# Kernel optimization log

Hardware: AMD Instinct MI355X
Metric: run time of the kernel (lower is better)

## Reference

```python
import jax, jax.numpy as jnp
import numpy as np

B, N, P = 8, 4096, 1024
P4 = P // 4
EPS = 1e-5


def _ln(x, g, b):
    mu = jnp.mean(x, axis=-1, keepdims=True)
    var = jnp.var(x, axis=-1, keepdims=True)
    return (x - mu) * jax.lax.rsqrt(var + EPS) * g + b


def setup_inputs() -> dict:
    key = jax.random.key(0)
    ks = jax.random.split(key, 16)
    s = lambda fan: 1.0 / np.sqrt(fan)
    return {
        "xyz": jax.random.normal(ks[0], (B, N, 3), jnp.float32),
        "x": jax.random.normal(ks[1], (B, N, P), jnp.float32),
        "ln1_g": jnp.ones((P,), jnp.float32),
        "ln1_b": jnp.zeros((P,), jnp.float32),
        "ln2_g": jnp.ones((P,), jnp.float32),
        "ln2_b": jnp.zeros((P,), jnp.float32),
        "qk_w": jax.random.normal(ks[2], (P4, P), jnp.float32) * s(P),   # shared q/k 1x1 conv, no bias
        "v_w": jax.random.normal(ks[3], (P, P), jnp.float32) * s(P),
        "v_b": jax.random.normal(ks[4], (P,), jnp.float32) * s(P),
        "t1_w": jax.random.normal(ks[5], (P, P4), jnp.float32) * s(P4),  # trans_conv
        "t1_b": jax.random.normal(ks[6], (P,), jnp.float32) * s(P4),
        "t2_w": jax.random.normal(ks[7], (P, P4), jnp.float32) * s(P4),  # trans_conv1
        "t2_b": jax.random.normal(ks[8], (P,), jnp.float32) * s(P4),
        "m1_w": jax.random.normal(ks[9], (P, P), jnp.float32) * s(P),
        "m1_b": jax.random.normal(ks[10], (P,), jnp.float32) * s(P),
        "m2_w": jax.random.normal(ks[11], (P, P), jnp.float32) * s(P),
        "m2_b": jax.random.normal(ks[12], (P,), jnp.float32) * s(P),
    }


def reference(xyz, x, ln1_g, ln1_b, ln2_g, ln2_b, qk_w, v_w, v_b,
              t1_w, t1_b, t2_w, t2_b, m1_w, m1_b, m2_w, m2_b):
    # xyz is accepted but unused, matching the torch module. Dropout = eval identity.
    res1 = x
    h = _ln(x, ln1_g, ln1_b)                                   # [B,N,P]
    # TransformerBlock_1 (1x1 convs on h^T [B,P,N] are just matmuls over P)
    x_q = jnp.einsum('op,bnp->bon', qk_w, h)                   # [B,P4,N]
    # k shares weights with q; x_k permuted is x_q transposed
    x_v = jnp.einsum('op,bnp->bno', v_w, h) + v_b              # [B,N,P]
    energy = jnp.einsum('bqn,bkn->bqk', x_q, x_q)              # [B,P4,P4]
    att = jnp.einsum('op,bpk->bok', t1_w, energy) + t1_b[:, None]   # [B,P,P4]
    att = jax.nn.gelu(att, approximate=False)
    att = jnp.einsum('op,bkp->bok', t2_w, att) + t2_b[:, None]      # [B,P,P]
    att = jax.nn.softmax(att, axis=-1)
    t_out = jnp.einsum('bnp,bpq->bnq', x_v, att)               # [B,N,P]
    x1 = t_out + res1
    h2 = _ln(x1, ln2_g, ln2_b)
    m = jax.nn.gelu(h2 @ m1_w.T + m1_b, approximate=False)
    m = m @ m2_w.T + m2_b
    return x1 + m
```

## Files before the change

kernel.cpp:

```cpp
#include <hip/hip_runtime.h>


typedef __attribute__((ext_vector_type(4))) float f32x4;
typedef __attribute__((ext_vector_type(8))) _Float16 h16x8;
typedef __attribute__((ext_vector_type(8))) unsigned short u16x8;
typedef __attribute__((ext_vector_type(4))) unsigned short u16x4;

__device__ __forceinline__ unsigned short f2h(float f) {
  _Float16 h = (_Float16)f;
  return __builtin_bit_cast(unsigned short, h);
}
__device__ __forceinline__ float h2f(unsigned short u) {
  return (float)__builtin_bit_cast(_Float16, u);
}
__device__ __forceinline__ unsigned split16(float f) {
  _Float16 h = (_Float16)f;
  _Float16 l = (_Float16)(f - (float)h);
  return (unsigned)__builtin_bit_cast(unsigned short, h) |
         ((unsigned)__builtin_bit_cast(unsigned short, l) << 16);
}
__device__ __forceinline__ float gelu_f(float x) {
  return 0.5f * x * (1.0f + erff(x * 0.70710678118654752f));
}
__device__ __forceinline__ void gload16(const void* g, void* l) {
  __builtin_amdgcn_global_load_lds(
      (const __attribute__((address_space(1))) unsigned int*)g,
      (__attribute__((address_space(3))) unsigned int*)l, 16, 0, 0);
}
#define FENCE() asm volatile("" ::: "memory")

__device__ __forceinline__ void xcd_swz(int& bx, int& by, int gx, int gy) {
  const int nwg = gx * gy;
  if ((nwg & 7) == 0 && nwg >= 16) {
    const int flat = bx + gx * by;
    const int chunk = nwg >> 3;
    const int nf = (flat & 7) * chunk + (flat >> 3);
    bx = nf % gx;
    by = nf / gx;
  }
}

__global__ __launch_bounds__(256)
void ln_kernel(const float* __restrict__ x, const float* __restrict__ g,
               const float* __restrict__ b, unsigned short* __restrict__ hi,
               unsigned short* __restrict__ lo, unsigned short* __restrict__ xh) {
  __shared__ float red[16];
  const size_t base = (size_t)blockIdx.x * 1024;
  const int t = threadIdx.x;
  f32x4 v = *(const f32x4*)&x[base + t * 4];
  float s = v[0] + v[1] + v[2] + v[3];
  float q = v[0] * v[0] + v[1] * v[1] + v[2] * v[2] + v[3] * v[3];
#pragma unroll
  for (int o = 32; o > 0; o >>= 1) { s += __shfl_down(s, o); q += __shfl_down(q, o); }
  const int w = t >> 6;
  if ((t & 63) == 0) { red[w] = s; red[8 + w] = q; }
  __syncthreads();
  s = (red[0] + red[1]) + (red[2] + red[3]);
  q = (red[8] + red[9]) + (red[10] + red[11]);
  const float mu = s * (1.0f / 1024.0f);
  const float var = q * (1.0f / 1024.0f) - mu * mu;
  const float is = rsqrtf(var + 1e-5f);
  f32x4 gg = *(const f32x4*)&g[t * 4];
  f32x4 bb = *(const f32x4*)&b[t * 4];
  u16x4 oh, ol, ox;
#pragma unroll
  for (int j = 0; j < 4; j++) {
    float y = (v[j] - mu) * is * gg[j] + bb[j];
    unsigned p = split16(y);
    oh[j] = (unsigned short)(p & 0xffffu);
    ol[j] = (unsigned short)(p >> 16);
    ox[j] = f2h(v[j]);
  }
  *(u16x4*)&hi[base + t * 4] = oh;
  if (lo) *(u16x4*)&lo[base + t * 4] = ol;
  if (xh) *(u16x4*)&xh[base + t * 4] = ox;
}

__global__ __launch_bounds__(256)
void stats16_kernel(const unsigned short* __restrict__ x16, float* __restrict__ muis) {
  __shared__ float red[16];
  const size_t base = (size_t)blockIdx.x * 1024;
  const int t = threadIdx.x;
  u16x4 raw = *(const u16x4*)&x16[base + t * 4];
  float v[4];
#pragma unroll
  for (int j = 0; j < 4; j++) v[j] = h2f(raw[j]);
  float s = v[0] + v[1] + v[2] + v[3];
  float q = v[0] * v[0] + v[1] * v[1] + v[2] * v[2] + v[3] * v[3];
#pragma unroll
  for (int o = 32; o > 0; o >>= 1) { s += __shfl_down(s, o); q += __shfl_down(q, o); }
  const int w = t >> 6;
  if ((t & 63) == 0) { red[w] = s; red[8 + w] = q; }
  __syncthreads();
  if (t == 0) {
    s = (red[0] + red[1]) + (red[2] + red[3]);
    q = (red[8] + red[9]) + (red[10] + red[11]);
    const float mu = s * (1.0f / 1024.0f);
    const float var = q * (1.0f / 1024.0f) - mu * mu;
    muis[blockIdx.x * 2] = mu;
    muis[blockIdx.x * 2 + 1] = rsqrtf(var + 1e-5f);
  }
}

__global__ __launch_bounds__(256)
void cvt_kernel(const float* __restrict__ in, unsigned short* __restrict__ hi,
                unsigned short* __restrict__ lo, int n4) {
  int i = blockIdx.x * 256 + threadIdx.x;
  if (i < n4) {
    f32x4 v = *(const f32x4*)&in[(size_t)i * 4];
    u16x4 oh, ol;
#pragma unroll
    for (int j = 0; j < 4; j++) {
      unsigned p = split16(v[j]);
      oh[j] = (unsigned short)(p & 0xffffu);
      ol[j] = (unsigned short)(p >> 16);
    }
    *(u16x4*)&hi[(size_t)i * 4] = oh;
    if (lo) *(u16x4*)&lo[(size_t)i * 4] = ol;
  }
}

__global__ __launch_bounds__(256)
void m1prep_kernel(const float* __restrict__ m1w, const float* __restrict__ lng,
                   const float* __restrict__ lnb, const float* __restrict__ m1b,
                   unsigned short* __restrict__ wp, float* __restrict__ S,
                   float* __restrict__ b2) {
  __shared__ float red[16];
  const int o = blockIdx.x;
  const int t = threadIdx.x;
  const float* row = m1w + (size_t)o * 1024;
  f32x4 wv = *(const f32x4*)&row[t * 4];
  f32x4 gv = *(const f32x4*)&lng[t * 4];
  f32x4 bv = *(const f32x4*)&lnb[t * 4];
  float s = 0.0f, d = 0.0f;
  u16x4 ow;
#pragma unroll
  for (int j = 0; j < 4; j++) {
    float wpj = wv[j] * gv[j];
    ow[j] = f2h(wpj);
    s += wpj;
    d += wv[j] * bv[j];
  }
  *(u16x4*)&wp[(size_t)o * 1024 + t * 4] = ow;
#pragma unroll
  for (int off = 32; off > 0; off >>= 1) { s += __shfl_down(s, off); d += __shfl_down(d, off); }
  const int w = t >> 6;
  if ((t & 63) == 0) { red[w] = s; red[8 + w] = d; }
  __syncthreads();
  if (t == 0) {
    S[o] = (red[0] + red[1]) + (red[2] + red[3]);
    b2[o] = m1b[o] + (red[8] + red[9]) + (red[10] + red[11]);
  }
}

__global__ __launch_bounds__(256)
void vwt_kernel(const float* __restrict__ vw, unsigned short* __restrict__ wvt) {
  __shared__ float T[64][65];
  const int bx = blockIdx.x, by = blockIdx.y;
  const int t = threadIdx.x;
  const int lr = t >> 6, lc = t & 63;
#pragma unroll
  for (int i = 0; i < 16; ++i) {
    const int row = i * 4 + lr;
    T[row][lc] = vw[(size_t)(by * 64 + row) * 1024 + bx * 64 + lc];
  }
  __syncthreads();
#pragma unroll
  for (int i = 0; i < 16; ++i) {
    const int row = i * 4 + lr;
    wvt[(size_t)(bx * 64 + row) * 1024 + by * 64 + lc] = f2h(T[lc][row]);
  }
}

__global__ __launch_bounds__(256)
void beff_kernel(const unsigned short* __restrict__ attT, const float* __restrict__ vb,
                 float* __restrict__ beff) {
  const int b = blockIdx.y;
  const int q = blockIdx.x * 4 + (threadIdx.x >> 6);
  const int l = threadIdx.x & 63;
  const unsigned short* row = attT + ((size_t)b * 1024 + q) * 1024;
  float s = 0.0f;
#pragma unroll
  for (int i = 0; i < 2; ++i) {
    u16x8 v = *(const u16x8*)&row[(i * 64 + l) * 8];
    f32x4 vb0 = *(const f32x4*)&vb[(i * 64 + l) * 8];
    f32x4 vb1 = *(const f32x4*)&vb[(i * 64 + l) * 8 + 4];
#pragma unroll
    for (int j = 0; j < 4; j++) s += h2f(v[j]) * vb0[j];
#pragma unroll
    for (int j = 0; j < 4; j++) s += h2f(v[j + 4]) * vb1[j];
  }
#pragma unroll
  for (int o = 32; o > 0; o >>= 1) s += __shfl_down(s, o);
  if (l == 0) beff[b * 1024 + q] = s;
}

template <int EPI>
__global__ __launch_bounds__(256)
void gemm_v(const unsigned short* __restrict__ Ain, const unsigned short* __restrict__ Bin,
            void* __restrict__ Cout, const float* __restrict__ bias,
            const unsigned short* __restrict__ res16In, const float* __restrict__ muis,
            const float* __restrict__ Svec,
            int K, int lda, int ldb, int ldc,
            long long sA, long long sB, long long sC, long long sBias, long long sRes) {
  __shared__ short As[2][4096];
  __shared__ short Bs[2][4096];
  const int z = blockIdx.z;
  const unsigned short* A = Ain + (size_t)z * sA;
  const unsigned short* B = Bin + (size_t)z * sB;
  int bx = blockIdx.x, by = blockIdx.y;
  xcd_swz(bx, by, gridDim.x, gridDim.y);
  const int mBase = by * 128, nBase = bx * 128;
  const int t = threadIdx.x, w = t >> 6, l = t & 63;
  const int r16 = l & 15, kq = l >> 4;
  const int wr = (w >> 1) * 64, wc = (w & 1) * 64;
  f32x4 acc[4][4] = {};

  auto stage = [&](int buf, int k0) {
#pragma unroll
    for (int i = 0; i < 2; ++i) {
      const int c = i * 256 + t;
      const int row = c >> 2, cc = c & 3;
      const int gc = cc ^ ((row >> 1) & 3);
      short* la = &As[buf][(i * 256 + w * 64) * 8];
      short* lb = &Bs[buf][(i * 256 + w * 64) * 8];
      gload16(&A[(size_t)(mBase + row) * lda + k0 + gc * 8], la);
      gload16(&B[(size_t)(nBase + row) * ldb + k0 + gc * 8], lb);
    }
  };

  const int nt = K >> 5;
  stage(0, 0);
  if (nt > 1) stage(1, 32);
  for (int ts = 0; ts < nt; ++ts) {
    const int cur = ts & 1;
    if (ts + 1 < nt) { asm volatile("s_waitcnt vmcnt(4)" ::: "memory"); }
    else             { asm volatile("s_waitcnt vmcnt(0)" ::: "memory"); }
    __builtin_amdgcn_s_barrier();
    FENCE();
    h16x8 aF[4], bF[4];
#pragma unroll
    for (int mi = 0; mi < 4; mi++) {
      const int r = wr + mi * 16 + r16;
      aF[mi] = *(const h16x8*)&As[cur][r * 32 + (kq ^ ((r >> 1) & 3)) * 8];
    }
#pragma unroll
    for (int ni = 0; ni < 4; ni++) {
      const int r = wc + ni * 16 + r16;
      bF[ni] = *(const h16x8*)&Bs[cur][r * 32 + (kq ^ ((r >> 1) & 3)) * 8];
    }
    __builtin_amdgcn_s_setprio(1);
#pragma unroll
    for (int mi = 0; mi < 4; mi++)
#pragma unroll
      for (int ni = 0; ni < 4; ni++)
        acc[mi][ni] = __builtin_amdgcn_mfma_f32_16x16x32_f16(aF[mi], bF[ni], acc[mi][ni], 0, 0, 0);
    __builtin_amdgcn_s_setprio(0);
    FENCE();
    __builtin_amdgcn_s_barrier();
    FENCE();
    if (ts + 2 < nt) stage(cur, (ts + 2) * 32);
  }
  FENCE();

  unsigned short* C16 = (unsigned short*)Cout + (size_t)z * sC;
  float* C32 = (float*)Cout + (size_t)z * sC;
  const float* bp = (EPI != 4) ? bias + (size_t)z * sBias : nullptr;
  const unsigned short* rp = (EPI == 3) ? res16In + (size_t)z * sRes : nullptr;

  if constexpr (EPI == 1 || EPI == 4 || EPI == 9) {
    short* ep = ((w & 2) ? &Bs[0][0] : &As[0][0]) + (w & 1) * 4096;
#pragma unroll
    for (int mi = 0; mi < 4; mi++) {
      float mu[4], is[4];
      if (EPI == 9) {
#pragma unroll
        for (int r = 0; r < 4; r++) {
          const int rw = mBase + wr + mi * 16 + kq * 4 + r;
          mu[r] = muis[rw * 2];
          is[r] = muis[rw * 2 + 1];
        }
      }
#pragma unroll
      for (int ni = 0; ni < 4; ni++) {
        const int cl = nBase + wc + ni * 16 + r16;
        const float bcol = bp ? bp[cl] : 0.0f;
        const float Scol = (EPI == 9) ? Svec[cl] : 0.0f;
#pragma unroll
        for (int r = 0; r < 4; r++) {
          float v;
          if (EPI == 9) v = gelu_f(is[r] * (acc[mi][ni][r] - mu[r] * Scol) + bcol);
          else {
            v = acc[mi][ni][r] + bcol;
            if (EPI == 1) v = gelu_f(v);
          }
          ep[(mi * 16 + kq * 4 + r) * 64 + ni * 16 + r16] = (short)f2h(v);
        }
      }
    }
#pragma unroll
    for (int j = 0; j < 8; j++) {
      const int f = j * 512 + l * 8;
      const int row = f >> 6, col = f & 63;
      const size_t gi = (size_t)(mBase + wr + row) * ldc + nBase + wc + col;
      *(u16x8*)&C16[gi] = *(const u16x8*)&ep[f];
    }
  } else {
#pragma unroll
    for (int mi = 0; mi < 4; mi++) {
#pragma unroll
      for (int ni = 0; ni < 4; ni++) {
        const int cl = nBase + wc + ni * 16 + r16;
        const float bcol = bp[cl];
#pragma unroll
        for (int r = 0; r < 4; r++) {
          const int rw = mBase + wr + mi * 16 + kq * 4 + r;
          const size_t idx = (size_t)rw * ldc + cl;
          C32[idx] = acc[mi][ni][r] + bcol + h2f(rp[idx]);
        }
      }
    }
  }
}

__global__ __launch_bounds__(256)
void gemm_r(const unsigned short* __restrict__ Ain, const unsigned short* __restrict__ Bin,
            unsigned short* __restrict__ Cout, const float* __restrict__ bias,
            const unsigned short* __restrict__ resIn,
            int K, int lda, int ldb, int ldc,
            long long sA, long long sB, long long sC, long long sBias, long long sRes) {
  __shared__ short As[2][4096];
  __shared__ short Bs[2][4096];
  const int z = blockIdx.z;
  const unsigned short* A = Ain + (size_t)z * sA;
  const unsigned short* B = Bin + (size_t)z * sB;
  int bx = blockIdx.x, by = blockIdx.y;
  xcd_swz(bx, by, gridDim.x, gridDim.y);
  const int mBase = by * 128, nBase = bx * 128;
  const int t = threadIdx.x, w = t >> 6, l = t & 63;
  const int r16 = l & 15, kq = l >> 4;
  const int wr = (w >> 1) * 64, wc = (w & 1) * 64;
  f32x4 acc[4][4] = {};

  const int row0 = t >> 2, row1 = 64 + (t >> 2);
  const int cc0 = t & 3;
  const int gc0 = cc0 ^ ((row0 >> 1) & 3);
  const int gc1 = cc0 ^ ((row1 >> 1) & 3);

  u16x8 ra0, ra1, rb0, rb1;
  auto loadreg = [&](int k0) {
    ra0 = *(const u16x8*)&A[(size_t)(mBase + row0) * lda + k0 + gc0 * 8];
    rb0 = *(const u16x8*)&B[(size_t)(nBase + row0) * ldb + k0 + gc0 * 8];
    ra1 = *(const u16x8*)&A[(size_t)(mBase + row1) * lda + k0 + gc1 * 8];
    rb1 = *(const u16x8*)&B[(size_t)(nBase + row1) * ldb + k0 + gc1 * 8];
  };
  auto dswrite = [&](int buf) {
    *(u16x8*)&As[buf][t * 8] = ra0;
    *(u16x8*)&Bs[buf][t * 8] = rb0;
    *(u16x8*)&As[buf][(256 + t) * 8] = ra1;
    *(u16x8*)&Bs[buf][(256 + t) * 8] = rb1;
  };

  const int nt = K >> 5;
  loadreg(0);
  dswrite(0);
  if (nt > 1) loadreg(32);
  asm volatile("s_waitcnt lgkmcnt(0)" ::: "memory");
  __builtin_amdgcn_s_barrier();
  FENCE();
  for (int ts = 0; ts < nt; ++ts) {
    const int cur = ts & 1;
    h16x8 aF[4], bF[4];
#pragma unroll
    for (int mi = 0; mi < 4; mi++) {
      const int r = wr + mi * 16 + r16;
      aF[mi] = *(const h16x8*)&As[cur][r * 32 + (kq ^ ((r >> 1) & 3)) * 8];
    }
#pragma unroll
    for (int ni = 0; ni < 4; ni++) {
      const int r = wc + ni * 16 + r16;
      bF[ni] = *(const h16x8*)&Bs[cur][r * 32 + (kq ^ ((r >> 1) & 3)) * 8];
    }
    __builtin_amdgcn_s_setprio(1);
#pragma unroll
    for (int mi = 0; mi < 4; mi++)
#pragma unroll
      for (int ni = 0; ni < 4; ni++)
        acc[mi][ni] = __builtin_amdgcn_mfma_f32_16x16x32_f16(aF[mi], bF[ni], acc[mi][ni], 0, 0, 0);
    __builtin_amdgcn_s_setprio(0);
    FENCE();
    if (ts + 1 < nt) {
      __builtin_amdgcn_s_barrier();
      FENCE();
      dswrite((ts + 1) & 1);
      if (ts + 2 < nt) loadreg((ts + 2) * 32);
      asm volatile("s_waitcnt lgkmcnt(0)" ::: "memory");
      FENCE();
      __builtin_amdgcn_s_barrier();
      FENCE();
    }
  }
  FENCE();

  unsigned short* C16 = Cout + (size_t)z * sC;
  const float* bp = bias + (size_t)z * sBias;
  const unsigned short* rp = resIn + (size_t)z * sRes;
  short* ep = ((w & 2) ? &Bs[0][0] : &As[0][0]) + (w & 1) * 4096;
#pragma unroll
  for (int mi = 0; mi < 4; mi++) {
#pragma unroll
    for (int ni = 0; ni < 4; ni++) {
      const int cl = nBase + wc + ni * 16 + r16;
      const float bcol = bp[cl];
#pragma unroll
      for (int r = 0; r < 4; r++)
        ep[(mi * 16 + kq * 4 + r) * 64 + ni * 16 + r16] =
            (short)f2h(acc[mi][ni][r] + bcol);
    }
  }
#pragma unroll
  for (int j = 0; j < 8; j++) {
    const int f = j * 512 + l * 8;
    const int row = f >> 6, col = f & 63;
    u16x8 v8 = *(const u16x8*)&ep[f];
    const size_t gi = (size_t)(mBase + wr + row) * ldc + nBase + wc + col;
    u16x8 r8 = *(const u16x8*)&rp[gi];
#pragma unroll
    for (int q = 0; q < 8; q++) v8[q] = f2h(h2f(v8[q]) + h2f(r8[q]));
    *(u16x8*)&C16[gi] = v8;
  }
}

template <int EPI, int SWAP>
__global__ __launch_bounds__(256)
void gemm_s(const unsigned short* __restrict__ Ahi, const unsigned short* __restrict__ Alo,
            const unsigned short* __restrict__ Bhi, const unsigned short* __restrict__ Blo,
            void* __restrict__ Cout, unsigned short* __restrict__ Cout2,
            const float* __restrict__ bias,
            int K, int lda, int ldb, int ldc,
            long long sA, long long sB, long long sC, int splitK) {
  __shared__ short As[2][8192];
  __shared__ short Bs[2][8192];
  const int z = blockIdx.z;
  const int bi = z / splitK, sp = z % splitK;
  const int kLen = K / splitK, kStart = sp * kLen;
  const unsigned short* AH = Ahi + (size_t)bi * sA;
  const unsigned short* BH = Bhi + (size_t)bi * sB;
  const unsigned short* AL = Alo + (size_t)bi * sA;
  const unsigned short* BL = Blo + (size_t)bi * sB;
  int bx = blockIdx.x, by = blockIdx.y;
  xcd_swz(bx, by, gridDim.x, gridDim.y);
  const int mBase = (SWAP ? bx : by) * 128, nBase = (SWAP ? by : bx) * 128;
  const int t = threadIdx.x, w = t >> 6, l = t & 63;
  const int r16 = l & 15, kq = l >> 4;
  const int wr = (w >> 1) * 64, wc = (w & 1) * 64;
  f32x4 acc[4][4] = {};

  auto stage = [&](int buf, int k0) {
#pragma unroll
    for (int i = 0; i < 2; ++i) {
      const int c = i * 256 + t;
      const int row = c >> 2, cc = c & 3;
      const int gc = cc ^ ((row >> 1) & 3);
      const int cbase = i * 256 + w * 64;
      const size_t ga = (size_t)(mBase + row) * lda + k0 + gc * 8;
      const size_t gb = (size_t)(nBase + row) * ldb + k0 + gc * 8;
      gload16(&AH[ga], &As[buf][cbase * 8]);
      gload16(&AL[ga], &As[buf][4096 + cbase * 8]);
      gload16(&BH[gb], &Bs[buf][cbase * 8]);
      gload16(&BL[gb], &Bs[buf][4096 + cbase * 8]);
    }
  };

  const int nsteps = kLen >> 5;
  stage(0, kStart);
  if (nsteps > 1) stage(1, kStart + 32);
  for (int ts = 0; ts < nsteps; ++ts) {
    const int cur = ts & 1;
    if (ts + 1 < nsteps) { asm volatile("s_waitcnt vmcnt(8)" ::: "memory"); }
    else                 { asm volatile("s_waitcnt vmcnt(0)" ::: "memory"); }
    __builtin_amdgcn_s_barrier();
    FENCE();
    h16x8 aH[4], bH[4], aL[4], bL[4];
#pragma unroll
    for (int mi = 0; mi < 4; mi++) {
      const int r = wr + mi * 16 + r16;
      const int off = r * 32 + (kq ^ ((r >> 1) & 3)) * 8;
      aH[mi] = *(const h16x8*)&As[cur][off];
      aL[mi] = *(const h16x8*)&As[cur][4096 + off];
    }
#pragma unroll
    for (int ni = 0; ni < 4; ni++) {
      const int r = wc + ni * 16 + r16;
      const int off = r * 32 + (kq ^ ((r >> 1) & 3)) * 8;
      bH[ni] = *(const h16x8*)&Bs[cur][off];
      bL[ni] = *(const h16x8*)&Bs[cur][4096 + off];
    }
    __builtin_amdgcn_s_setprio(1);
#pragma unroll
    for (int mi = 0; mi < 4; mi++)
#pragma unroll
      for (int ni = 0; ni < 4; ni++) {
        acc[mi][ni] = __builtin_amdgcn_mfma_f32_16x16x32_f16(aH[mi], bH[ni], acc[mi][ni], 0, 0, 0);
        acc[mi][ni] = __builtin_amdgcn_mfma_f32_16x16x32_f16(aH[mi], bL[ni], acc[mi][ni], 0, 0, 0);
        acc[mi][ni] = __builtin_amdgcn_mfma_f32_16x16x32_f16(aL[mi], bH[ni], acc[mi][ni], 0, 0, 0);
      }
    __builtin_amdgcn_s_setprio(0);
    FENCE();
    __builtin_amdgcn_s_barrier();
    FENCE();
    if (ts + 2 < nsteps) stage(cur, kStart + (ts + 2) * 32);
  }
  FENCE();

  unsigned short* C16 = (unsigned short*)Cout + (size_t)z * sC;
  unsigned short* C16b = Cout2 ? Cout2 + (size_t)z * sC : nullptr;
  float* C32 = (float*)Cout + (size_t)z * sC;

  if constexpr (EPI == 4 || EPI == 6) {
    short* ep = &As[0][0] + w * 4096;
    unsigned pk[4][4][4];
#pragma unroll
    for (int mi = 0; mi < 4; mi++)
#pragma unroll
      for (int ni = 0; ni < 4; ni++)
#pragma unroll
        for (int r = 0; r < 4; r++) {
          float v = acc[mi][ni][r];
          if (EPI == 6) { v += bias[mBase + wr + mi * 16 + kq * 4 + r]; v = gelu_f(v); }
          pk[mi][ni][r] = split16(v);
        }
#pragma unroll
    for (int mi = 0; mi < 4; mi++)
#pragma unroll
      for (int ni = 0; ni < 4; ni++)
#pragma unroll
        for (int r = 0; r < 4; r++)
          ep[(mi * 16 + kq * 4 + r) * 64 + ni * 16 + r16] =
              (short)(pk[mi][ni][r] & 0xffffu);
#pragma unroll
    for (int j = 0; j < 8; j++) {
      const int f = j * 512 + l * 8;
      const int row = f >> 6, col = f & 63;
      *(u16x8*)&C16[(size_t)(mBase + wr + row) * ldc + nBase + wc + col] =
          *(const u16x8*)&ep[f];
    }
#pragma unroll
    for (int mi = 0; mi < 4; mi++)
#pragma unroll
      for (int ni = 0; ni < 4; ni++)
#pragma unroll
        for (int r = 0; r < 4; r++)
          ep[(mi * 16 + kq * 4 + r) * 64 + ni * 16 + r16] =
              (short)(pk[mi][ni][r] >> 16);
#pragma unroll
    for (int j = 0; j < 8; j++) {
      const int f = j * 512 + l * 8;
      const int row = f >> 6, col = f & 63;
      *(u16x8*)&C16b[(size_t)(mBase + wr + row) * ldc + nBase + wc + col] =
          *(const u16x8*)&ep[f];
    }
  } else {
#pragma unroll
    for (int mi = 0; mi < 4; mi++) {
#pragma unroll
      for (int ni = 0; ni < 4; ni++) {
        const int cl = nBase + wc + ni * 16 + r16;
#pragma unroll
        for (int r = 0; r < 4; r++) {
          const int rw = mBase + wr + mi * 16 + kq * 4 + r;
          float v = acc[mi][ni][r];
          if (EPI == 7) v += bias[rw];
          C32[(size_t)rw * ldc + cl] = v;
        }
      }
    }
  }
}

__global__ __launch_bounds__(256)
void ereduce_kernel(const float* __restrict__ part, unsigned short* __restrict__ ehi,
                    unsigned short* __restrict__ elo) {
  const size_t idx = (size_t)blockIdx.x * 256 + threadIdx.x;
  const size_t b = idx >> 16, i = idx & 65535;
  const float* p = part + b * (8ull * 65536) + i;
  float s0 = (p[0] + p[65536]) + (p[2 * 65536] + p[3 * 65536]);
  float s1 = (p[4 * 65536] + p[5 * 65536]) + (p[6 * 65536] + p[7 * 65536]);
  unsigned pk = split16(s0 + s1);
  ehi[idx] = (unsigned short)(pk & 0xffffu);
  elo[idx] = (unsigned short)(pk >> 16);
}

__global__ __launch_bounds__(256)
void smax_t_kernel(const float* __restrict__ a2, unsigned short* __restrict__ attT) {
  __shared__ float S[8][1028];
  __shared__ float inv[8];
  const int t = threadIdx.x;
  const int b = blockIdx.y;
  const int o0 = blockIdx.x * 8;
  const float* src = a2 + ((size_t)b * 1024 + o0) * 1024;
#pragma unroll
  for (int i = 0; i < 8; i++)
    *(f32x4*)&S[i][t * 4] = *(const f32x4*)&src[(size_t)i * 1024 + t * 4];
  __syncthreads();
  const int w = t >> 6, l = t & 63;
  for (int rr = 0; rr < 2; rr++) {
    const int r = w * 2 + rr;
    float m = -1e30f;
#pragma unroll
    for (int i = 0; i < 16; i++) m = fmaxf(m, S[r][l + i * 64]);
#pragma unroll
    for (int o = 32; o > 0; o >>= 1) m = fmaxf(m, __shfl_xor(m, o));
    float ssum = 0.0f;
#pragma unroll
    for (int i = 0; i < 16; i++) {
      float e = expf(S[r][l + i * 64] - m);
      S[r][l + i * 64] = e;
      ssum += e;
    }
#pragma unroll
    for (int o = 32; o > 0; o >>= 1) ssum += __shfl_xor(ssum, o);
    if (l == 0) inv[r] = 1.0f / ssum;
  }
  __syncthreads();
  float iv[8];
#pragma unroll
  for (int r = 0; r < 8; r++) iv[r] = inv[r];
#pragma unroll
  for (int i = 0; i < 4; i++) {
    const int k = i * 256 + t;
    u16x8 ov;
#pragma unroll
    for (int r = 0; r < 8; r++) ov[r] = f2h(S[r][k] * iv[r]);
    *(u16x8*)&attT[((size_t)b * 1024 + k) * 1024 + o0] = ov;
  }
}

extern "C" void kernel_launch(void* const* d_in, const int* in_sizes, int n_in,
                              void* d_out, int out_size, void* d_ws, size_t ws_size,
                              hipStream_t stream) {
  (void)in_sizes; (void)n_in; (void)out_size; (void)ws_size;
  const float* x     = (const float*)d_in[1];
  const float* ln1_g = (const float*)d_in[2];
  const float* ln1_b = (const float*)d_in[3];
  const float* ln2_g = (const float*)d_in[4];
  const float* ln2_b = (const float*)d_in[5];
  const float* qk_w  = (const float*)d_in[6];
  const float* v_w   = (const float*)d_in[7];
  const float* v_b   = (const float*)d_in[8];
  const float* t1_w  = (const float*)d_in[9];
  const float* t1_b  = (const float*)d_in[10];
  const float* t2_w  = (const float*)d_in[11];
  const float* t2_b  = (const float*)d_in[12];
  const float* m1_w  = (const float*)d_in[13];
  const float* m1_b  = (const float*)d_in[14];
  const float* m2_w  = (const float*)d_in[15];
  const float* m2_b  = (const float*)d_in[16];

  char* ws = (char*)d_ws;
  unsigned short* hhi  = (unsigned short*)(ws + 0);
  unsigned short* hlo  = (unsigned short*)(ws + 67108864);
  unsigned short* Qthi = (unsigned short*)(ws + 134217728);
  unsigned short* Qtlo = (unsigned short*)(ws + 150994944);
  float*          part = (float*)(ws + 167772160);
  unsigned short* Ehi  = (unsigned short*)(ws + 184549376);
  unsigned short* Elo  = (unsigned short*)(ws + 185597952);
  unsigned short* Ghi  = (unsigned short*)(ws + 186646528);
  unsigned short* Glo  = (unsigned short*)(ws + 190840832);
  float*          a2   = (float*)(ws + 195035136);
  unsigned short* attT = (unsigned short*)(ws + 228589568);
  unsigned short* WeT  = (unsigned short*)(ws + 245366784);
  float*          beff = (float*)(ws + 262144000);
  float*          muis = (float*)(ws + 262176768);
  float*          Svec = (float*)(ws + 262438912);
  float*          b2   = (float*)(ws + 262443008);
  unsigned short* xh   = (unsigned short*)(ws + 268435456);
  unsigned short* x1h  = (unsigned short*)(ws + 335544320);
  unsigned short* wqh  = (unsigned short*)(ws + 446693376);
  unsigned short* wql  = (unsigned short*)(ws + 447217664);
  unsigned short* wvt  = (unsigned short*)(ws + 447741952);
  unsigned short* wt1h = (unsigned short*)(ws + 449839104);
  unsigned short* wt1l = (unsigned short*)(ws + 450363392);
  unsigned short* wt2h = (unsigned short*)(ws + 450887680);
  unsigned short* wt2l = (unsigned short*)(ws + 451411968);
  unsigned short* wm1p = (unsigned short*)(ws + 451936256);
  unsigned short* wm2  = (unsigned short*)(ws + 454033408);
  unsigned short* gb = hlo;
  float* out = (float*)d_out;

  cvt_kernel<<<dim3(256),  dim3(256), 0, stream>>>(qk_w, wqh, wql, 65536);
  vwt_kernel<<<dim3(16, 16), dim3(256), 0, stream>>>(v_w, wvt);
  cvt_kernel<<<dim3(256),  dim3(256), 0, stream>>>(t1_w, wt1h, wt1l, 65536);
  cvt_kernel<<<dim3(256),  dim3(256), 0, stream>>>(t2_w, wt2h, wt2l, 65536);
  m1prep_kernel<<<dim3(1024), dim3(256), 0, stream>>>(m1_w, ln2_g, ln2_b, m1_b, wm1p, Svec, b2);
  cvt_kernel<<<dim3(1024), dim3(256), 0, stream>>>(m2_w, wm2, nullptr, 262144);
  ln_kernel<<<dim3(32768), dim3(256), 0, stream>>>(x, ln1_g, ln1_b, hhi, hlo, xh);
  gemm_s<4, 1><<<dim3(2, 32, 8), dim3(256), 0, stream>>>(
      wqh, wql, hhi, hlo, Qthi, Qtlo, nullptr,
      1024, 1024, 1024, 4096, 0, 4194304, 1048576, 1);
  gemm_s<5, 0><<<dim3(2, 2, 64), dim3(256), 0, stream>>>(
      Qthi, Qtlo, Qthi, Qtlo, part, nullptr, nullptr,
      4096, 4096, 4096, 256, 1048576, 1048576, 65536, 8);
  ereduce_kernel<<<dim3(2048), dim3(256), 0, stream>>>(part, Ehi, Elo);
  gemm_s<6, 0><<<dim3(2, 8, 8), dim3(256), 0, stream>>>(
      wt1h, wt1l, Ehi, Elo, Ghi, Glo, t1_b,
      256, 256, 256, 256, 0, 65536, 262144, 1);
  gemm_s<7, 0><<<dim3(8, 8, 8), dim3(256), 0, stream>>>(
      wt2h, wt2l, Ghi, Glo, a2, nullptr, t2_b,
      256, 256, 256, 1024, 0, 262144, 1048576, 1);
  smax_t_kernel<<<dim3(128, 8), dim3(256), 0, stream>>>(a2, attT);
  gemm_v<4><<<dim3(8, 8, 8), dim3(256), 0, stream>>>(
      attT, wvt, WeT, nullptr, nullptr, nullptr, nullptr,
      1024, 1024, 1024, 1024, 1048576, 0, 1048576, 0, 0);
  beff_kernel<<<dim3(256, 8), dim3(256), 0, stream>>>(attT, v_b, beff);
  gemm_r<<<dim3(8, 32, 8), dim3(256), 0, stream>>>(
      hhi, WeT, x1h, beff, xh,
      1024, 1024, 1024, 1024, 4194304, 1048576, 4194304, 1024, 4194304);
  stats16_kernel<<<dim3(32768), dim3(256), 0, stream>>>(x1h, muis);
  gemm_v<9><<<dim3(8, 256, 1), dim3(256), 0, stream>>>(
      x1h, wm1p, gb, b2, nullptr, muis, Svec,
      1024, 1024, 1024, 1024, 0, 0, 0, 0, 0);
  gemm_v<3><<<dim3(8, 256, 1), dim3(256), 0, stream>>>(
      gb, wm2, out, m2_b, x1h, nullptr, nullptr,
      1024, 1024, 1024, 1024, 0, 0, 0, 0, 0);
}
```

Before: 634.8 us.

## Fold LayerNorm1 into Q and V GEMM epilogues via per-row stats

Replaces the materialized LN1 output with a raw split-fp16 copy of x plus per-row mean/inv-std, folding gamma into the Q and V weights and applying mean/scale corrections in the GEMM epilogues. The separate fp16 copy of x used as residual is dropped, and the residual now reads from the hi half of x. This removes writing the LN output and the xh buffer. The trade-off is extra epilogue arithmetic, extra prep kernels, and possible precision loss from cancellation in the mean-subtraction done after the matmul.

```diff
diff --git a/kernel.cpp b/kernel.cpp
--- a/kernel.cpp
+++ b/kernel.cpp
@@ -41,9 +41,8 @@
 }
 
 __global__ __launch_bounds__(256)
-void ln_kernel(const float* __restrict__ x, const float* __restrict__ g,
-               const float* __restrict__ b, unsigned short* __restrict__ hi,
-               unsigned short* __restrict__ lo, unsigned short* __restrict__ xh) {
+void lnsplit_kernel(const float* __restrict__ x, unsigned short* __restrict__ xhi,
+                    unsigned short* __restrict__ xlo, float* __restrict__ muis) {
   __shared__ float red[16];
   const size_t base = (size_t)blockIdx.x * 1024;
   const int t = threadIdx.x;
@@ -54,26 +53,24 @@
   for (int o = 32; o > 0; o >>= 1) { s += __shfl_down(s, o); q += __shfl_down(q, o); }
   const int w = t >> 6;
   if ((t & 63) == 0) { red[w] = s; red[8 + w] = q; }
-  __syncthreads();
-  s = (red[0] + red[1]) + (red[2] + red[3]);
-  q = (red[8] + red[9]) + (red[10] + red[11]);
-  const float mu = s * (1.0f / 1024.0f);
-  const float var = q * (1.0f / 1024.0f) - mu * mu;
-  const float is = rsqrtf(var + 1e-5f);
-  f32x4 gg = *(const f32x4*)&g[t * 4];
-  f32x4 bb = *(const f32x4*)&b[t * 4];
-  u16x4 oh, ol, ox;
+  u16x4 oh, ol;
 #pragma unroll
   for (int j = 0; j < 4; j++) {
-    float y = (v[j] - mu) * is * gg[j] + bb[j];
-    unsigned p = split16(y);
+    unsigned p = split16(v[j]);
     oh[j] = (unsigned short)(p & 0xffffu);
     ol[j] = (unsigned short)(p >> 16);
-    ox[j] = f2h(v[j]);
-  }
-  *(u16x4*)&hi[base + t * 4] = oh;
-  if (lo) *(u16x4*)&lo[base + t * 4] = ol;
-  if (xh) *(u16x4*)&xh[base + t * 4] = ox;
+  }
+  *(u16x4*)&xhi[base + t * 4] = oh;
+  *(u16x4*)&xlo[base + t * 4] = ol;
+  __syncthreads();
+  if (t == 0) {
+    s = (red[0] + red[1]) + (red[2] + red[3]);
+    q = (red[8] + red[9]) + (red[10] + red[11]);
+    const float mu = s * (1.0f / 1024.0f);
+    const float var = q * (1.0f / 1024.0f) - mu * mu;
+    muis[blockIdx.x * 2] = mu;
+    muis[blockIdx.x * 2 + 1] = rsqrtf(var + 1e-5f);
+  }
 }
 
 __global__ __launch_bounds__(256)
@@ -117,6 +114,42 @@
     }
     *(u16x4*)&hi[(size_t)i * 4] = oh;
     if (lo) *(u16x4*)&lo[(size_t)i * 4] = ol;
+  }
+}
+
+__global__ __launch_bounds__(256)
+void wqprep_kernel(const float* __restrict__ qkw, const float* __restrict__ lng,
+                   const float* __restrict__ lnb, unsigned short* __restrict__ wh,
+                   unsigned short* __restrict__ wl, float* __restrict__ S,
+                   float* __restrict__ B0) {
+  __shared__ float red[16];
+  const int o = blockIdx.x;
+  const int t = threadIdx.x;
+  const float* row = qkw + (size_t)o * 1024;
+  f32x4 wv = *(const f32x4*)&row[t * 4];
+  f32x4 gv = *(const f32x4*)&lng[t * 4];
+  f32x4 bv = *(const f32x4*)&lnb[t * 4];
+  float s = 0.0f, d = 0.0f;
+  u16x4 oh, ol;
+#pragma unroll
+  for (int j = 0; j < 4; j++) {
+    float wg = wv[j] * gv[j];
+    unsigned p = split16(wg);
+    oh[j] = (unsigned short)(p & 0xffffu);
+    ol[j] = (unsigned short)(p >> 16);
+    s += wg;
+    d += wv[j] * bv[j];
+  }
+  *(u16x4*)&wh[(size_t)o * 1024 + t * 4] = oh;
+  *(u16x4*)&wl[(size_t)o * 1024 + t * 4] = ol;
+#pragma unroll
+  for (int off = 32; off > 0; off >>= 1) { s += __shfl_down(s, off); d += __shfl_down(d, off); }
+  const int w = t >> 6;
+  if ((t & 63) == 0) { red[w] = s; red[8 + w] = d; }
+  __syncthreads();
+  if (t == 0) {
+    S[o] = (red[0] + red[1]) + (red[2] + red[3]);
+    B0[o] = (red[8] + red[9]) + (red[10] + red[11]);
   }
 }
 
@@ -154,7 +187,33 @@
 }
 
 __global__ __launch_bounds__(256)
-void vwt_kernel(const float* __restrict__ vw, unsigned short* __restrict__ wvt) {
+void vwvec_kernel(const float* __restrict__ vw, const float* __restrict__ lng,
+                  const float* __restrict__ lnb, const float* __restrict__ vb,
+                  float* __restrict__ gv, float* __restrict__ vb2) {
+  __shared__ float red[16];
+  const int p = blockIdx.x;
+  const int t = threadIdx.x;
+  const float* row = vw + (size_t)p * 1024;
+  f32x4 wv = *(const f32x4*)&row[t * 4];
+  f32x4 gg = *(const f32x4*)&lng[t * 4];
+  f32x4 bb = *(const f32x4*)&lnb[t * 4];
+  float s = 0.0f, d = 0.0f;
+#pragma unroll
+  for (int j = 0; j < 4; j++) { s += wv[j] * gg[j]; d += wv[j] * bb[j]; }
+#pragma unroll
+  for (int off = 32; off > 0; off >>= 1) { s += __shfl_down(s, off); d += __shfl_down(d, off); }
+  const int w = t >> 6;
+  if ((t & 63) == 0) { red[w] = s; red[8 + w] = d; }
+  __syncthreads();
+  if (t == 0) {
+    gv[p] = (red[0] + red[1]) + (red[2] + red[3]);
+    vb2[p] = vb[p] + (red[8] + red[9]) + (red[10] + red[11]);
+  }
+}
+
+__global__ __launch_bounds__(256)
+void vwt_kernel(const float* __restrict__ vw, const float* __restrict__ lng,
+                unsigned short* __restrict__ wvt) {
   __shared__ float T[64][65];
   const int bx = blockIdx.x, by = blockIdx.y;
   const int t = threadIdx.x;
@@ -168,31 +227,34 @@
 #pragma unroll
   for (int i = 0; i < 16; ++i) {
     const int row = i * 4 + lr;
-    wvt[(size_t)(bx * 64 + row) * 1024 + by * 64 + lc] = f2h(T[lc][row]);
-  }
-}
-
-__global__ __launch_bounds__(256)
-void beff_kernel(const unsigned short* __restrict__ attT, const float* __restrict__ vb,
-                 float* __restrict__ beff) {
+    wvt[(size_t)(bx * 64 + row) * 1024 + by * 64 + lc] =
+        f2h(T[lc][row] * lng[bx * 64 + row]);
+  }
+}
+
+__global__ __launch_bounds__(256)
+void attdots_kernel(const unsigned short* __restrict__ attT, const float* __restrict__ vb2,
+                    const float* __restrict__ gv, float* __restrict__ add1,
+                    float* __restrict__ Sg) {
   const int b = blockIdx.y;
   const int q = blockIdx.x * 4 + (threadIdx.x >> 6);
   const int l = threadIdx.x & 63;
   const unsigned short* row = attT + ((size_t)b * 1024 + q) * 1024;
-  float s = 0.0f;
+  float s = 0.0f, d = 0.0f;
 #pragma unroll
   for (int i = 0; i < 2; ++i) {
     u16x8 v = *(const u16x8*)&row[(i * 64 + l) * 8];
-    f32x4 vb0 = *(const f32x4*)&vb[(i * 64 + l) * 8];
-    f32x4 vb1 = *(const f32x4*)&vb[(i * 64 + l) * 8 + 4];
-#pragma unroll
-    for (int j = 0; j < 4; j++) s += h2f(v[j]) * vb0[j];
-#pragma unroll
-    for (int j = 0; j < 4; j++) s += h2f(v[j + 4]) * vb1[j];
-  }
-#pragma unroll
-  for (int o = 32; o > 0; o >>= 1) s += __shfl_down(s, o);
-  if (l == 0) beff[b * 1024 + q] = s;
+#pragma unroll
+    for (int j = 0; j < 8; j++) {
+      const float a = h2f(v[j]);
+      const int idx = (i * 64 + l) * 8 + j;
+      s += a * vb2[idx];
+      d += a * gv[idx];
+    }
+  }
+#pragma unroll
+  for (int o = 32; o > 0; o >>= 1) { s += __shfl_down(s, o); d += __shfl_down(d, o); }
+  if (l == 0) { add1[b * 1024 + q] = s; Sg[b * 1024 + q] = d; }
 }
 
 template <int EPI>
@@ -325,10 +387,11 @@
 
 __global__ __launch_bounds__(256)
 void gemm_r(const unsigned short* __restrict__ Ain, const unsigned short* __restrict__ Bin,
-            unsigned short* __restrict__ Cout, const float* __restrict__ bias,
+            unsigned short* __restrict__ Cout, const float* __restrict__ muis,
+            const float* __restrict__ SgIn, const float* __restrict__ add1In,
             const unsigned short* __restrict__ resIn,
             int K, int lda, int ldb, int ldc,
-            long long sA, long long sB, long long sC, long long sBias, long long sRes) {
+            long long sA, long long sB, long long sC, long long sRes) {
   __shared__ short As[2][4096];
   __shared__ short Bs[2][4096];
   const int z = blockIdx.z;
@@ -403,19 +466,29 @@
   FENCE();
 
   unsigned short* C16 = Cout + (size_t)z * sC;
-  const float* bp = bias + (size_t)z * sBias;
+  const float* muz = muis + (size_t)z * 8192;
+  const float* Sg = SgIn + (size_t)z * 1024;
+  const float* ad = add1In + (size_t)z * 1024;
   const unsigned short* rp = resIn + (size_t)z * sRes;
   short* ep = ((w & 2) ? &Bs[0][0] : &As[0][0]) + (w & 1) * 4096;
 #pragma unroll
   for (int mi = 0; mi < 4; mi++) {
+    float mu[4], is[4];
+#pragma unroll
+    for (int r = 0; r < 4; r++) {
+      const int rw = mBase + wr + mi * 16 + kq * 4 + r;
+      mu[r] = muz[rw * 2];
+      is[r] = muz[rw * 2 + 1];
+    }
 #pragma unroll
     for (int ni = 0; ni < 4; ni++) {
       const int cl = nBase + wc + ni * 16 + r16;
-      const float bcol = bp[cl];
+      const float sgc = Sg[cl];
+      const float adc = ad[cl];
 #pragma unroll
       for (int r = 0; r < 4; r++)
         ep[(mi * 16 + kq * 4 + r) * 64 + ni * 16 + r16] =
-            (short)f2h(acc[mi][ni][r] + bcol);
+            (short)f2h(is[r] * (acc[mi][ni][r] - mu[r] * sgc) + adc);
     }
   }
 #pragma unroll
@@ -436,7 +509,8 @@
 void gemm_s(const unsigned short* __restrict__ Ahi, const unsigned short* __restrict__ Alo,
             const unsigned short* __restrict__ Bhi, const unsigned short* __restrict__ Blo,
             void* __restrict__ Cout, unsigned short* __restrict__ Cout2,
-            const float* __restrict__ bias,
+            const float* __restrict__ bias, const float* __restrict__ B0vec,
+            const float* __restrict__ mu1,
             int K, int lda, int ldb, int ldc,
             long long sA, long long sB, long long sC, int splitK) {
   __shared__ short As[2][8192];
@@ -517,19 +591,29 @@
   unsigned short* C16b = Cout2 ? Cout2 + (size_t)z * sC : nullptr;
   float* C32 = (float*)Cout + (size_t)z * sC;
 
-  if constexpr (EPI == 4 || EPI == 6) {
+  if constexpr (EPI == 6 || EPI == 10) {
     short* ep = &As[0][0] + w * 4096;
+    const float* mu1b = (EPI == 10) ? mu1 + (size_t)bi * 8192 : nullptr;
     unsigned pk[4][4][4];
 #pragma unroll
     for (int mi = 0; mi < 4; mi++)
 #pragma unroll
-      for (int ni = 0; ni < 4; ni++)
+      for (int ni = 0; ni < 4; ni++) {
+        float muc = 0.f, isc = 0.f;
+        if (EPI == 10) {
+          const int cl = nBase + wc + ni * 16 + r16;
+          muc = mu1b[cl * 2];
+          isc = mu1b[cl * 2 + 1];
+        }
 #pragma unroll
         for (int r = 0; r < 4; r++) {
+          const int rw = mBase + wr + mi * 16 + kq * 4 + r;
           float v = acc[mi][ni][r];
-          if (EPI == 6) { v += bias[mBase + wr + mi * 16 + kq * 4 + r]; v = gelu_f(v); }
+          if (EPI == 6) { v += bias[rw]; v = gelu_f(v); }
+          if (EPI == 10) v = isc * (v - muc * bias[rw]) + B0vec[rw];
           pk[mi][ni][r] = split16(v);
         }
+      }
 #pragma unroll
     for (int mi = 0; mi < 4; mi++)
 #pragma unroll
@@ -658,8 +742,8 @@
   const float* m2_b  = (const float*)d_in[16];
 
   char* ws = (char*)d_ws;
-  unsigned short* hhi  = (unsigned short*)(ws + 0);
-  unsigned short* hlo  = (unsigned short*)(ws + 67108864);
+  unsigned short* xhi  = (unsigned short*)(ws + 0);
+  unsigned short* xlo  = (unsigned short*)(ws + 67108864);
   unsigned short* Qthi = (unsigned short*)(ws + 134217728);
   unsigned short* Qtlo = (unsigned short*)(ws + 150994944);
   float*          part = (float*)(ws + 167772160);
@@ -670,11 +754,16 @@
   float*          a2   = (float*)(ws + 195035136);
   unsigned short* attT = (unsigned short*)(ws + 228589568);
   unsigned short* WeT  = (unsigned short*)(ws + 245366784);
-  float*          beff = (float*)(ws + 262144000);
-  float*          muis = (float*)(ws + 262176768);
-  float*          Svec = (float*)(ws + 262438912);
-  float*          b2   = (float*)(ws + 262443008);
-  unsigned short* xh   = (unsigned short*)(ws + 268435456);
+  float*          add1 = (float*)(ws + 262144000);
+  float*          Sg   = (float*)(ws + 262176768);
+  float*          muis1= (float*)(ws + 262209536);
+  float*          muis2= (float*)(ws + 262471680);
+  float*          SvM1 = (float*)(ws + 262733824);
+  float*          b2   = (float*)(ws + 262737920);
+  float*          SQt  = (float*)(ws + 262742016);
+  float*          B0Qt = (float*)(ws + 262746112);
+  float*          gv   = (float*)(ws + 262750208);
+  float*          vb2  = (float*)(ws + 262754304);
   unsigned short* x1h  = (unsigned short*)(ws + 335544320);
   unsigned short* wqh  = (unsigned short*)(ws + 446693376);
   unsigned short* wql  = (unsigned short*)(ws + 447217664);
@@ -685,40 +774,41 @@
   unsigned short* wt2l = (unsigned short*)(ws + 451411968);
   unsigned short* wm1p = (unsigned short*)(ws + 451936256);
   unsigned short* wm2  = (unsigned short*)(ws + 454033408);
-  unsigned short* gb = hlo;
+  unsigned short* gb = xlo;
   float* out = (float*)d_out;
 
-  cvt_kernel<<<dim3(256),  dim3(256), 0, stream>>>(qk_w, wqh, wql, 65536);
-  vwt_kernel<<<dim3(16, 16), dim3(256), 0, stream>>>(v_w, wvt);
+  wqprep_kernel<<<dim3(256), dim3(256), 0, stream>>>(qk_w, ln1_g, ln1_b, wqh, wql, SQt, B0Qt);
+  vwt_kernel<<<dim3(16, 16), dim3(256), 0, stream>>>(v_w, ln1_g, wvt);
+  vwvec_kernel<<<dim3(1024), dim3(256), 0, stream>>>(v_w, ln1_g, ln1_b, v_b, gv, vb2);
   cvt_kernel<<<dim3(256),  dim3(256), 0, stream>>>(t1_w, wt1h, wt1l, 65536);
   cvt_kernel<<<dim3(256),  dim3(256), 0, stream>>>(t2_w, wt2h, wt2l, 65536);
-  m1prep_kernel<<<dim3(1024), dim3(256), 0, stream>>>(m1_w, ln2_g, ln2_b, m1_b, wm1p, Svec, b2);
+  m1prep_kernel<<<dim3(1024), dim3(256), 0, stream>>>(m1_w, ln2_g, ln2_b, m1_b, wm1p, SvM1, b2);
   cvt_kernel<<<dim3(1024), dim3(256), 0, stream>>>(m2_w, wm2, nullptr, 262144);
-  ln_kernel<<<dim3(32768), dim3(256), 0, stream>>>(x, ln1_g, ln1_b, hhi, hlo, xh);
-  gemm_s<4, 1><<<dim3(2, 32, 8), dim3(256), 0, stream>>>(
-      wqh, wql, hhi, hlo, Qthi, Qtlo, nullptr,
+  lnsplit_kernel<<<dim3(32768), dim3(256), 0, stream>>>(x, xhi, xlo, muis1);
+  gemm_s<10, 1><<<dim3(2, 32, 8), dim3(256), 0, stream>>>(
+      wqh, wql, xhi, xlo, Qthi, Qtlo, SQt, B0Qt, muis1,
       1024, 1024, 1024, 4096, 0, 4194304, 1048576, 1);
   gemm_s<5, 0><<<dim3(2, 2, 64), dim3(256), 0, stream>>>(
-      Qthi, Qtlo, Qthi, Qtlo, part, nullptr, nullptr,
+      Qthi, Qtlo, Qthi, Qtlo, part, nullptr, nullptr, nullptr, nullptr,
       4096, 4096, 4096, 256, 1048576, 1048576, 65536, 8);
   ereduce_kernel<<<dim3(2048), dim3(256), 0, stream>>>(part, Ehi, Elo);
   gemm_s<6, 0><<<dim3(2, 8, 8), dim3(256), 0, stream>>>(
-      wt1h, wt1l, Ehi, Elo, Ghi, Glo, t1_b,
+      wt1h, wt1l, Ehi, Elo, Ghi, Glo, t1_b, nullptr, nullptr,
       256, 256, 256, 256, 0, 65536, 262144, 1);
   gemm_s<7, 0><<<dim3(8, 8, 8), dim3(256), 0, stream>>>(
-      wt2h, wt2l, Ghi, Glo, a2, nullptr, t2_b,
+      wt2h, wt2l, Ghi, Glo, a2, nullptr, t2_b, nullptr, nullptr,
       256, 256, 256, 1024, 0, 262144, 1048576, 1);
   smax_t_kernel<<<dim3(128, 8), dim3(256), 0, stream>>>(a2, attT);
   gemm_v<4><<<dim3(8, 8, 8), dim3(256), 0, stream>>>(
       attT, wvt, WeT, nullptr, nullptr, nullptr, nullptr,
       1024, 1024, 1024, 1024, 1048576, 0, 1048576, 0, 0);
-  beff_kernel<<<dim3(256, 8), dim3(256), 0, stream>>>(attT, v_b, beff);
+  attdots_kernel<<<dim3(256, 8), dim3(256), 0, stream>>>(attT, vb2, gv, add1, Sg);
   gemm_r<<<dim3(8, 32, 8), dim3(256), 0, stream>>>(
-      hhi, WeT, x1h, beff, xh,
-      1024, 1024, 1024, 1024, 4194304, 1048576, 4194304, 1024, 4194304);
-  stats16_kernel<<<dim3(32768), dim3(256), 0, stream>>>(x1h, muis);
+      xhi, WeT, x1h, muis1, Sg, add1, xhi,
+      1024, 1024, 1024, 1024, 4194304, 1048576, 4194304, 4194304);
+  stats16_kernel<<<dim3(32768), dim3(256), 0, stream>>>(x1h, muis2);
   gemm_v<9><<<dim3(8, 256, 1), dim3(256), 0, stream>>>(
-      x1h, wm1p, gb, b2, nullptr, muis, Svec,
+      x1h, wm1p, gb, b2, nullptr, muis2, SvM1,
       1024, 1024, 1024, 1024, 0, 0, 0, 0, 0);
   gemm_v<3><<<dim3(8, 256, 1), dim3(256), 0, stream>>>(
       gb, wm2, out, m2_b, x1h, nullptr, nullptr,
```

Result: no change. 633.0 us (-0.3%).
